# Kernel tuning notes

Hardware: AMD Instinct MI355X
Metric: run time of the kernel (lower is better)

Reference implementation:

```python
import math
import jax, jax.numpy as jnp
import numpy as np

C, H, W = 128, 64, 64
R, K = 7, 3          # 7x3 dilated window
PAD_H, PAD_W = 9, 2  # from unfold paddings
DIL_H, DIL_W = 3, 2  # row/col dilations


def _neighborhood(x):
    """Gather dilated 7x3 neighborhood: out[n,c,r,k,i,j] = x[n,c, i+3r-9, j+2k-2] (zero-padded).
    x: (n,c,h,w) -> (n,c,7,3,h,w)."""
    n, c, h, w = x.shape
    xp = jnp.pad(x, ((0, 0), (0, 0), (PAD_H, PAD_H), (PAD_W, PAD_W)))
    taps = [xp[:, :, DIL_H * r:DIL_H * r + h, DIL_W * k:DIL_W * k + w]
            for r in range(R) for k in range(K)]
    return jnp.stack(taps, axis=2).reshape(n, c, R, K, h, w)


def setup_inputs() -> dict:
    key = jax.random.key(0)
    k1, k2, k3 = jax.random.split(key, 3)
    x = jax.random.normal(k1, (4, C, H, W), dtype=jnp.float32)
    p5_w = 0.1 * jax.random.normal(k2, (1, C, R, K, H, W), dtype=jnp.float32)
    p6_w = 0.1 * jax.random.normal(k3, (1, C, R, K, C), dtype=jnp.float32)
    return {"x": x, "p5_w": p5_w, "p6_w": p6_w}


def reference(x, p5_w, p6_w):
    n, c, h, w = x.shape
    # t_2: dilated 7x3 neighborhood gather (double unfold)
    t2 = _neighborhood(x)                                   # (n,c,7,3,h,w)
    # t_3: bmm((n,c*21,hw), (n,hw,c)) / sqrt(hw)
    t3 = jnp.einsum('ncrkhw,ndhw->ncrkd', t2, x) / math.sqrt(h * w)  # (n,c,7,3,c)
    # elementwise modulation
    t7 = p5_w * t2 + t2                                     # (n,c,7,3,h,w)
    t6 = p6_w * t3                                          # (n,c,7,3,c)
    # t_8: bmm((n,hw,c*21), (n,c*21,c)) / sqrt(c*21)
    t8 = jnp.einsum('ncrkhw,ncrkd->nhwd', t7, t6) / math.sqrt(c * R * K)  # (n,h,w,c)
    return jnp.transpose(t8, (0, 3, 1, 2))                  # (n,c,h,w)
```

## Files before the change

### kernel.cpp

```cpp
#include <hip/hip_runtime.h>

typedef _Float16 f16;
typedef _Float16 f16x2 __attribute__((ext_vector_type(2)));
typedef _Float16 f16x4 __attribute__((ext_vector_type(4)));
typedef _Float16 f16x8 __attribute__((ext_vector_type(8)));
typedef float    f32x4 __attribute__((ext_vector_type(4)));

#define XROWS 82
#define XSTR  (XROWS * 64)
#define XK_ELEMS (3u * 4u * 128u * (unsigned)XSTR)
static const size_t T6T_OFF   = (size_t)XK_ELEMS * 2;
static const size_t T6T_BYTES = (size_t)4 * 128 * 2688 * 2;
static const size_t T3P_OFF   = T6T_OFF + T6T_BYTES;
static const size_t T8P_OFF   = T3P_OFF;

__device__ __forceinline__ void gl16(const f16* g, f16* l) {
  __builtin_amdgcn_global_load_lds((const __attribute__((address_space(1))) void*)g,
                                   (__attribute__((address_space(3))) void*)l, 16, 0, 0);
}

__global__ __launch_bounds__(256) void prep_kernel(const float* __restrict__ x,
                                                   f16* __restrict__ xk) {
  unsigned p = blockIdx.x * 256u + threadIdx.x;
  unsigned wseg = p & 7u;
  unsigned row  = (p >> 3) % 82u;
  unsigned rest = p / (8u * 82u);
  unsigned c    = rest & 127u;
  unsigned rest2 = rest >> 7;
  unsigned n    = rest2 & 3u;
  unsigned kc   = rest2 >> 2;
  int hsrc = (int)row - 9;
  int wb   = (int)(wseg * 8u) + 2 * (int)kc - 2;
  f16x8 v = {};
  if (hsrc >= 0 && hsrc < 64) {
    const float* srow = x + ((size_t)(n * 128u + c) * 64u + (unsigned)hsrc) * 64u;
#pragma unroll
    for (int i = 0; i < 4; i++) {
      int ws = wb + 2 * i;
      if (ws >= 0 && ws < 64) {
        float2 xv = *(const float2*)(srow + ws);
        v[2 * i]     = (f16)(xv.x * 0.125f);
        v[2 * i + 1] = (f16)(xv.y * 0.125f);
      }
    }
  }
  *(f16x8*)(xk + (size_t)p * 8u) = v;
}

__global__ __launch_bounds__(256, 3) void gram_kernel(const f16* __restrict__ xk,
                                                      f16* __restrict__ t3p) {
  __shared__ f16 gl[2 * 12288];

  unsigned b    = blockIdx.x;
  unsigned ks   = b & 7u;
  unsigned cseg = (b >> 3) & 1u;
  unsigned rki  = (b >> 4) % 11u;
  unsigned n    = b / 176u;
  unsigned r    = rki / 3u;
  unsigned kc   = rki - r * 3u;

  unsigned tid  = threadIdx.x;
  unsigned wv   = tid >> 6;
  unsigned lane = tid & 63u;
  unsigned wy   = wv >> 1;
  unsigned wx   = wv & 1u;
  unsigned quad = lane >> 4;
  unsigned l16  = lane & 15u;
  unsigned rsl  = lane >> 3;
  unsigned seg  = (lane & 7u) ^ (rsl & 7u);

  unsigned h0 = ks * 8u;
  const f16* Ab = xk + (size_t)(kc * 4u + n) * 128u * XSTR + (size_t)(cseg * 64u) * XSTR
                + (h0 + 3u * r) * 64u + seg * 8u;
  const f16* Bb = xk + (size_t)(4u + n) * 128u * XSTR + (h0 + 9u) * 64u + seg * 8u;
  unsigned ar0 = wv * 16u;
  unsigned br0 = wv * 32u;

  f32x4 acc[2][4] = {};

#pragma unroll
  for (unsigned t = 0; t < 2u; t++)
    gl16(Ab + (size_t)(ar0 + t * 8u + rsl) * XSTR, &gl[(ar0 + t * 8u) * 64u]);
#pragma unroll
  for (unsigned t = 0; t < 4u; t++)
    gl16(Bb + (size_t)(br0 + t * 8u + rsl) * XSTR, &gl[4096u + (br0 + t * 8u) * 64u]);

  for (unsigned s = 0; s < 8u; s++) {
    __syncthreads();
    if (s < 7u) {
      f16* base = &gl[((s + 1u) & 1u) * 12288u];
      unsigned off = (s + 1u) * 64u;
#pragma unroll
      for (unsigned t = 0; t < 2u; t++)
        gl16(Ab + off + (size_t)(ar0 + t * 8u + rsl) * XSTR, base + (ar0 + t * 8u) * 64u);
#pragma unroll
      for (unsigned t = 0; t < 4u; t++)
        gl16(Bb + off + (size_t)(br0 + t * 8u + rsl) * XSTR, base + 4096u + (br0 + t * 8u) * 64u);
    }
    const f16* bufA = &gl[(s & 1u) * 12288u];
    const f16* bufB = bufA + 4096u;
#pragma unroll
    for (unsigned t2 = 0; t2 < 2u; t2++) {
      unsigned L = t2 * 4u + quad;
      f16x8 a[2], bb[4];
#pragma unroll
      for (int ms = 0; ms < 2; ms++) {
        unsigned rr = wy * 32u + (unsigned)ms * 16u + l16;
        a[ms] = *(const f16x8*)&bufA[rr * 64u + (L ^ (rr & 7u)) * 8u];
      }
#pragma unroll
      for (int ns = 0; ns < 4; ns++) {
        unsigned rb = wx * 64u + (unsigned)ns * 16u + l16;
        bb[ns] = *(const f16x8*)&bufB[rb * 64u + (L ^ (rb & 7u)) * 8u];
      }
#pragma unroll
      for (int ms = 0; ms < 2; ms++)
#pragma unroll
        for (int ns = 0; ns < 4; ns++)
          acc[ms][ns] = __builtin_amdgcn_mfma_f32_16x16x32_f16(a[ms], bb[ns], acc[ms][ns], 0, 0, 0);
    }
  }

  f16* tp = t3p + ((size_t)(ks * 4u + n) * 11u + rki) * 16384u;
#pragma unroll
  for (int ms = 0; ms < 2; ms++) {
#pragma unroll
    for (int ns = 0; ns < 4; ns++) {
      unsigned c0 = cseg * 64u + wy * 32u + (unsigned)ms * 16u + quad * 4u;
      unsigned d  = wx * 64u + (unsigned)ns * 16u + l16;
#pragma unroll
      for (int reg = 0; reg < 4; reg++)
        tp[(size_t)(c0 + (unsigned)reg) * 128u + d] = (f16)acc[ms][ns][reg];
    }
  }
}

__global__ __launch_bounds__(256) void ep_kernel(const f16* __restrict__ t3p,
                                                 const float* __restrict__ p6,
                                                 f16* __restrict__ t6B) {
  unsigned idx = blockIdx.x * 256u + threadIdx.x;
  unsigned d4 = idx & 31u;
  unsigned c  = (idx >> 5) & 127u;
  unsigned t  = idx >> 12;
  unsigned rk = t % 11u;
  unsigned n  = t / 11u;
  unsigned d0 = d4 * 4u;

  float s0 = 0.f, s1 = 0.f, s2 = 0.f, s3 = 0.f;
#pragma unroll
  for (unsigned ks = 0; ks < 8u; ks++) {
    f16x4 v = *(const f16x4*)(t3p + (((size_t)(ks * 4u + n) * 11u + rk) * 16384u + c * 128u + d0));
    s0 += (float)v[0]; s1 += (float)v[1]; s2 += (float)v[2]; s3 += (float)v[3];
  }

  const float* pp = p6 + ((size_t)c * 21u + rk) * 128u + d0;
  f16* ob = t6B + (size_t)(n * 21u + rk) * 16384u
          + (c >> 5) * 4096u + (d0 >> 4) * 512u + ((c >> 3) & 3u) * 128u + (d0 & 15u) * 8u + (c & 7u);
  ob[0]  = (f16)(s0 * pp[0]);
  ob[8]  = (f16)(s1 * pp[1]);
  ob[16] = (f16)(s2 * pp[2]);
  ob[24] = (f16)(s3 * pp[3]);

  if (rk < 10u) {
    unsigned rk2 = 20u - rk;
    f16x4 o;
    o[0] = (f16)(s0 * p6[(size_t)(d0 + 0u) * 2688u + rk2 * 128u + c]);
    o[1] = (f16)(s1 * p6[(size_t)(d0 + 1u) * 2688u + rk2 * 128u + c]);
    o[2] = (f16)(s2 * p6[(size_t)(d0 + 2u) * 2688u + rk2 * 128u + c]);
    o[3] = (f16)(s3 * p6[(size_t)(d0 + 3u) * 2688u + rk2 * 128u + c]);
    f16* mb = t6B + (size_t)(n * 21u + rk2) * 16384u
            + (d0 >> 5) * 4096u + (c >> 4) * 512u + ((d0 >> 3) & 3u) * 128u + (c & 15u) * 8u + (d0 & 7u);
    *(f16x4*)mb = o;
  }
}

#define RT_STR   66
__global__ __launch_bounds__(512, 8) void outp_kernel(const f16* __restrict__ xk,
                                                      const float* __restrict__ p5,
                                                      const f16* __restrict__ t6B,
                                                      f16* __restrict__ t8p) {
  __shared__ float smem[8448];
  f16* sm16 = (f16*)smem;

  unsigned b = blockIdx.x;
  unsigned g = b & 3u;
  unsigned h = (b >> 2) & 63u;
  unsigned n = b >> 8;

  unsigned tid  = threadIdx.x;
  unsigned wv   = tid >> 6;
  unsigned lane = tid & 63u;
  unsigned wy   = wv >> 2;
  unsigned wx   = wv & 3u;
  unsigned quad = lane >> 4;
  unsigned l16  = lane & 15u;
  unsigned wst  = tid & 63u;
  unsigned cg4  = tid >> 6;
  unsigned cth  = g * 32u + cg4 * 4u;
  unsigned gr8  = cg4 >> 1;
  unsigned sub  = cg4 & 1u;

  const float* prow0 = p5 + (size_t)cth * (21u * 4096u) + h * 64u + wst;
  const f16* t6base = t6B + (size_t)n * 344064u + g * 4096u;

  f32x4 acc[2][2] = {};
  f16 xv[4]; float pv[4];

  {
    const f16* xrow = xk + (((size_t)n * 128u + cth) * XROWS + h) * 64u + wst;
#pragma unroll
    for (int i = 0; i < 4; i++) { xv[i] = xrow[(size_t)i * XSTR]; pv[i] = prow0[(size_t)i * (21u * 4096u)]; }
    gl16(t6base + (size_t)tid * 8u, sm16 + 4096u + tid * 8u);
  }

  for (unsigned j = 0; j < 21u; j++) {
    f16* Ag = sm16 + (j & 1u) * 2048u;
    const f16* Bg = sm16 + 4096u + (j & 1u) * 4096u;
    {
      f16x4 av;
#pragma unroll
      for (int i = 0; i < 4; i++) av[i] = (f16)((float)xv[i] * (1.0f + pv[i]));
      unsigned gw = ((wst & 1u) << 2) | gr8;
      *(f16x4*)&Ag[(wst >> 1) * 64u + (gw ^ ((wst >> 1) & 7u)) * 8u + sub * 4u] = av;
    }
    __syncthreads();

    if (j < 20u) {
      unsigned rk = j + 1u;
      gl16(t6base + (size_t)rk * 16384u + tid * 8u,
           sm16 + 4096u + (rk & 1u) * 4096u + tid * 8u);
      unsigned rr = rk / 3u;
      unsigned kcc = rk - rr * 3u;
      const f16* xrow = xk + (((size_t)(kcc * 4u + n) * 128u + cth) * XROWS + (h + 3u * rr)) * 64u + wst;
      const float* prow = prow0 + rk * 4096u;
#pragma unroll
      for (int i = 0; i < 4; i++) { xv[i] = xrow[(size_t)i * XSTR]; pv[i] = prow[(size_t)i * (21u * 4096u)]; }
    }

    f16x8 a[2], bfr[2];
#pragma unroll
    for (int ms = 0; ms < 2; ms++) {
      unsigned rr = wy * 32u + (unsigned)ms * 16u + l16;
      unsigned gr2 = ((rr & 1u) << 2) | quad;
      a[ms] = *(const f16x8*)&Ag[(rr >> 1) * 64u + (gr2 ^ ((rr >> 1) & 7u)) * 8u];
    }
#pragma unroll
    for (int ns = 0; ns < 2; ns++)
      bfr[ns] = *(const f16x8*)&Bg[(wx * 2u + (unsigned)ns) * 512u + lane * 8u];
#pragma unroll
    for (int ms = 0; ms < 2; ms++)
#pragma unroll
      for (int ns = 0; ns < 2; ns++)
        acc[ms][ns] = __builtin_amdgcn_mfma_f32_16x16x32_f16(a[ms], bfr[ns], acc[ms][ns], 0, 0, 0);
  }

  __syncthreads();
  float* Rt = smem;
#pragma unroll
  for (int ms = 0; ms < 2; ms++)
#pragma unroll
    for (int ns = 0; ns < 2; ns++) {
      unsigned w0 = wy * 32u + (unsigned)ms * 16u + quad * 4u;
      unsigned d  = wx * 32u + (unsigned)ns * 16u + l16;
#pragma unroll
      for (int reg = 0; reg < 4; reg++)
        Rt[d * RT_STR + w0 + (unsigned)reg] = acc[ms][ns][reg];
    }
  __syncthreads();
  f16* op = t8p + ((size_t)((g * 4u + n) * 64u + h)) * 8192u;
  {
    unsigned row = tid >> 2;
    unsigned w0  = (tid & 3u) * 16u;
    f16x8 o0, o1;
#pragma unroll
    for (int i = 0; i < 8; i++) {
      o0[i] = (f16)Rt[row * RT_STR + w0 + (unsigned)i];
      o1[i] = (f16)Rt[row * RT_STR + w0 + 8u + (unsigned)i];
    }
    *(f16x8*)(op + row * 64u + w0) = o0;
    *(f16x8*)(op + row * 64u + w0 + 8u) = o1;
  }
}

__global__ __launch_bounds__(256) void red_kernel(const f16* __restrict__ t8p,
                                                  float* __restrict__ out) {
  unsigned idx = blockIdx.x * 256u + threadIdx.x;
  unsigned w0 = (idx & 7u) * 8u;
  unsigned h  = (idx >> 3) & 63u;
  unsigned d  = (idx >> 9) & 127u;
  unsigned n  = idx >> 16;
  const float FS = 0.15430334996209192f;
  float s[8] = {};
#pragma unroll
  for (unsigned g = 0; g < 4u; g++) {
    f16x8 v = *(const f16x8*)(t8p + ((size_t)((g * 4u + n) * 64u + h)) * 8192u + d * 64u + w0);
#pragma unroll
    for (int i = 0; i < 8; i++) s[i] += (float)v[i];
  }
  f32x4 o0, o1;
#pragma unroll
  for (int i = 0; i < 4; i++) { o0[i] = s[i] * FS; o1[i] = s[i + 4] * FS; }
  float* op = out + ((size_t)(n * 128u + d) * 64u + h) * 64u + w0;
  *(f32x4*)op = o0;
  *(f32x4*)(op + 4) = o1;
}

extern "C" void kernel_launch(void* const* d_in, const int* in_sizes, int n_in,
                              void* d_out, int out_size, void* d_ws, size_t ws_size,
                              hipStream_t stream) {
  const float* x  = (const float*)d_in[0];
  const float* p5 = (const float*)d_in[1];
  const float* p6 = (const float*)d_in[2];
  float* out = (float*)d_out;
  f16* xk  = (f16*)((char*)d_ws);
  f16* t6B = (f16*)((char*)d_ws + T6T_OFF);
  f16* t3p = (f16*)((char*)d_ws + T3P_OFF);
  f16* t8p = (f16*)((char*)d_ws + T8P_OFF);

  hipLaunchKernelGGL(prep_kernel, dim3(3936), dim3(256), 0, stream, x, xk);
  hipLaunchKernelGGL(gram_kernel, dim3(704),  dim3(256), 0, stream, xk, t3p);
  hipLaunchKernelGGL(ep_kernel,   dim3(704),  dim3(256), 0, stream, t3p, p6, t6B);
  hipLaunchKernelGGL(outp_kernel, dim3(1024), dim3(512), 0, stream, xk, p5, t6B, t8p);
  hipLaunchKernelGGL(red_kernel,  dim3(1024), dim3(256), 0, stream, t8p, out);
}
```

Baseline: 145.0 us.

## Process two rk taps per barrier in outp_kernel with deeper LDS buffering

The outp_kernel main loop now handles an even and an odd tap per iteration, running 11 iterations instead of 21. Two A tiles and two B tiles are staged per step, and the B ring grows to four slots. This roughly halves the number of __syncthreads barriers and puts more loads in flight per barrier. In exchange it raises LDS use from about 33KB to 48KB and lowers the occupancy hint from 8 to 6, and the extra prefetch registers add register pressure.

```diff
diff --git a/kernel.cpp b/kernel.cpp
--- a/kernel.cpp
+++ b/kernel.cpp
@@ -175,11 +175,11 @@
 }
 
 #define RT_STR   66
-__global__ __launch_bounds__(512, 8) void outp_kernel(const f16* __restrict__ xk,
+__global__ __launch_bounds__(512, 6) void outp_kernel(const f16* __restrict__ xk,
                                                       const float* __restrict__ p5,
                                                       const f16* __restrict__ t6B,
                                                       f16* __restrict__ t8p) {
-  __shared__ float smem[8448];
+  __shared__ float smem[12288];
   f16* sm16 = (f16*)smem;
 
   unsigned b = blockIdx.x;
@@ -199,59 +199,105 @@
   unsigned cth  = g * 32u + cg4 * 4u;
   unsigned gr8  = cg4 >> 1;
   unsigned sub  = cg4 & 1u;
+  unsigned gw   = ((wst & 1u) << 2) | gr8;
+  unsigned awoff = (wst >> 1) * 64u + (gw ^ ((wst >> 1) & 7u)) * 8u + sub * 4u;
 
   const float* prow0 = p5 + (size_t)cth * (21u * 4096u) + h * 64u + wst;
   const f16* t6base = t6B + (size_t)n * 344064u + g * 4096u;
 
   f32x4 acc[2][2] = {};
-  f16 xv[4]; float pv[4];
+  f16 xvE[4], xvO[4]; float pvE[4], pvO[4];
 
   {
-    const f16* xrow = xk + (((size_t)n * 128u + cth) * XROWS + h) * 64u + wst;
-#pragma unroll
-    for (int i = 0; i < 4; i++) { xv[i] = xrow[(size_t)i * XSTR]; pv[i] = prow0[(size_t)i * (21u * 4096u)]; }
-    gl16(t6base + (size_t)tid * 8u, sm16 + 4096u + tid * 8u);
-  }
-
-  for (unsigned j = 0; j < 21u; j++) {
-    f16* Ag = sm16 + (j & 1u) * 2048u;
-    const f16* Bg = sm16 + 4096u + (j & 1u) * 4096u;
+    gl16(t6base + (size_t)tid * 8u, sm16 + 8192u + tid * 8u);
+    gl16(t6base + 16384u + (size_t)tid * 8u, sm16 + 8192u + 4096u + tid * 8u);
+    const f16* xr0 = xk + (((size_t)n * 128u + cth) * XROWS + h) * 64u + wst;
+    const f16* xr1 = xk + (((size_t)(1u * 4u + n) * 128u + cth) * XROWS + h) * 64u + wst;
+#pragma unroll
+    for (int i = 0; i < 4; i++) {
+      xvE[i] = xr0[(size_t)i * XSTR]; pvE[i] = prow0[(size_t)i * (21u * 4096u)];
+      xvO[i] = xr1[(size_t)i * XSTR]; pvO[i] = prow0[4096u + (size_t)i * (21u * 4096u)];
+    }
+  }
+
+  for (unsigned it = 0; it < 11u; it++) {
+    unsigned pr = it & 1u;
+    f16* AgE = sm16 + (pr * 2u) * 2048u;
+    f16* AgO = AgE + 2048u;
+    bool hasOdd = (it < 10u);
     {
       f16x4 av;
 #pragma unroll
-      for (int i = 0; i < 4; i++) av[i] = (f16)((float)xv[i] * (1.0f + pv[i]));
-      unsigned gw = ((wst & 1u) << 2) | gr8;
-      *(f16x4*)&Ag[(wst >> 1) * 64u + (gw ^ ((wst >> 1) & 7u)) * 8u + sub * 4u] = av;
+      for (int i = 0; i < 4; i++) av[i] = (f16)((float)xvE[i] * (1.0f + pvE[i]));
+      *(f16x4*)&AgE[awoff] = av;
+      if (hasOdd) {
+        f16x4 ao;
+#pragma unroll
+        for (int i = 0; i < 4; i++) ao[i] = (f16)((float)xvO[i] * (1.0f + pvO[i]));
+        *(f16x4*)&AgO[awoff] = ao;
+      }
     }
     __syncthreads();
 
-    if (j < 20u) {
-      unsigned rk = j + 1u;
-      gl16(t6base + (size_t)rk * 16384u + tid * 8u,
-           sm16 + 4096u + (rk & 1u) * 4096u + tid * 8u);
-      unsigned rr = rk / 3u;
-      unsigned kcc = rk - rr * 3u;
-      const f16* xrow = xk + (((size_t)(kcc * 4u + n) * 128u + cth) * XROWS + (h + 3u * rr)) * 64u + wst;
-      const float* prow = prow0 + rk * 4096u;
-#pragma unroll
-      for (int i = 0; i < 4; i++) { xv[i] = xrow[(size_t)i * XSTR]; pv[i] = prow[(size_t)i * (21u * 4096u)]; }
-    }
-
-    f16x8 a[2], bfr[2];
-#pragma unroll
-    for (int ms = 0; ms < 2; ms++) {
-      unsigned rr = wy * 32u + (unsigned)ms * 16u + l16;
-      unsigned gr2 = ((rr & 1u) << 2) | quad;
-      a[ms] = *(const f16x8*)&Ag[(rr >> 1) * 64u + (gr2 ^ ((rr >> 1) & 7u)) * 8u];
-    }
-#pragma unroll
-    for (int ns = 0; ns < 2; ns++)
-      bfr[ns] = *(const f16x8*)&Bg[(wx * 2u + (unsigned)ns) * 512u + lane * 8u];
-#pragma unroll
-    for (int ms = 0; ms < 2; ms++)
+    if (it < 10u) {
+      unsigned rkE = 2u * it + 2u;
+      gl16(t6base + (size_t)rkE * 16384u + tid * 8u,
+           sm16 + 8192u + (rkE & 3u) * 4096u + tid * 8u);
+      {
+        unsigned rr = rkE / 3u, kcc = rkE - rr * 3u;
+        const f16* xrow = xk + (((size_t)(kcc * 4u + n) * 128u + cth) * XROWS + (h + 3u * rr)) * 64u + wst;
+        const float* prow = prow0 + rkE * 4096u;
+#pragma unroll
+        for (int i = 0; i < 4; i++) { xvE[i] = xrow[(size_t)i * XSTR]; pvE[i] = prow[(size_t)i * (21u * 4096u)]; }
+      }
+      unsigned rkO = 2u * it + 3u;
+      if (rkO < 21u) {
+        gl16(t6base + (size_t)rkO * 16384u + tid * 8u,
+             sm16 + 8192u + (rkO & 3u) * 4096u + tid * 8u);
+        unsigned rr = rkO / 3u, kcc = rkO - rr * 3u;
+        const f16* xrow = xk + (((size_t)(kcc * 4u + n) * 128u + cth) * XROWS + (h + 3u * rr)) * 64u + wst;
+        const float* prow = prow0 + rkO * 4096u;
+#pragma unroll
+        for (int i = 0; i < 4; i++) { xvO[i] = xrow[(size_t)i * XSTR]; pvO[i] = prow[(size_t)i * (21u * 4096u)]; }
+      }
+    }
+
+    {
+      const f16* Bg = sm16 + 8192u + ((2u * it) & 3u) * 4096u;
+      f16x8 a[2], bfr[2];
+#pragma unroll
+      for (int ms = 0; ms < 2; ms++) {
+        unsigned rr = wy * 32u + (unsigned)ms * 16u + l16;
+        unsigned gr2 = ((rr & 1u) << 2) | quad;
+        a[ms] = *(const f16x8*)&AgE[(rr >> 1) * 64u + (gr2 ^ ((rr >> 1) & 7u)) * 8u];
+      }
 #pragma unroll
       for (int ns = 0; ns < 2; ns++)
-        acc[ms][ns] = __builtin_amdgcn_mfma_f32_16x16x32_f16(a[ms], bfr[ns], acc[ms][ns], 0, 0, 0);
+        bfr[ns] = *(const f16x8*)&Bg[(wx * 2u + (unsigned)ns) * 512u + lane * 8u];
+#pragma unroll
+      for (int ms = 0; ms < 2; ms++)
+#pragma unroll
+        for (int ns = 0; ns < 2; ns++)
+          acc[ms][ns] = __builtin_amdgcn_mfma_f32_16x16x32_f16(a[ms], bfr[ns], acc[ms][ns], 0, 0, 0);
+    }
+    if (hasOdd) {
+      const f16* Bg = sm16 + 8192u + ((2u * it + 1u) & 3u) * 4096u;
+      f16x8 a[2], bfr[2];
+#pragma unroll
+      for (int ms = 0; ms < 2; ms++) {
+        unsigned rr = wy * 32u + (unsigned)ms * 16u + l16;
+        unsigned gr2 = ((rr & 1u) << 2) | quad;
+        a[ms] = *(const f16x8*)&AgO[(rr >> 1) * 64u + (gr2 ^ ((rr >> 1) & 7u)) * 8u];
+      }
+#pragma unroll
+      for (int ns = 0; ns < 2; ns++)
+        bfr[ns] = *(const f16x8*)&Bg[(wx * 2u + (unsigned)ns) * 512u + lane * 8u];
+#pragma unroll
+      for (int ms = 0; ms < 2; ms++)
+#pragma unroll
+        for (int ns = 0; ns < 2; ns++)
+          acc[ms][ns] = __builtin_amdgcn_mfma_f32_16x16x32_f16(a[ms], bfr[ns], acc[ms][ns], 0, 0, 0);
+    }
   }
 
   __syncthreads();
```

Measured after the change: 149.2 us. +2.9%, slower.
